# Optimization experiments

Hardware: AMD Instinct MI355X
Metric: run time of the kernel (lower is better)

Reference implementation:

```python
import jax, jax.numpy as jnp
import numpy as np

TEMP = 0.5
NUM_QUERIES = 256
NUM_NEGATIVES = 256
STRONG_THRESHOLD = 0.97


def _l2norm(x):
    n = jnp.sqrt(jnp.sum(x * x, axis=-1, keepdims=True))
    return x / jnp.maximum(n, 1e-12)


def _mls(mu0, mu1, s0, s1, w0, w1):
    # mutual likelihood score, mean over feature dim
    mu0 = _l2norm(mu0)
    mu1 = _l2norm(mu1)
    up = (mu0 * w0 - mu1 * w1) ** 2
    down = s0 * w0 + s1 * w1
    return -0.5 * jnp.mean(up / down + jnp.log(down), axis=-1)


def setup_inputs() -> dict:
    key = jax.random.key(0)
    B, C, H, W, S = 4, 32, 256, 256, 8
    ks = jax.random.split(key, 6)
    weights = jax.random.uniform(ks[0], (B, C, H, W), jnp.float32, 0.1, 1.0)
    mu = jax.random.normal(ks[1], (B, C, H, W), jnp.float32)
    sigma = jax.random.uniform(ks[2], (B, C, H, W), jnp.float32, 0.1, 1.0)
    cls = jax.random.randint(ks[3], (B, H, W), 0, S)
    label = jax.nn.one_hot(cls, S, axis=1, dtype=jnp.float32)  # [B,S,H,W]
    mask = (jax.random.uniform(ks[4], (B, 1, H, W)) < 0.7).astype(jnp.float32)
    prob = jax.random.uniform(ks[5], (B, S, H, W), jnp.float32)
    return {"weights": weights, "mu": mu, "sigma": sigma, "label": label, "mask": mask, "prob": prob}


def _rank_table(m, N):
    # m: bool [S, N]. table[s, r] = pixel index with rank r within class s.
    S = m.shape[0]
    ranks = jnp.cumsum(m, axis=1) - 1
    idx = jnp.where(m, ranks, N)  # out-of-range entries are dropped
    tbl = jnp.zeros((S, N), jnp.int32)
    rows = jnp.broadcast_to(jnp.arange(S)[:, None], (S, N))
    vals = jnp.broadcast_to(jnp.arange(N, dtype=jnp.int32)[None, :], (S, N))
    return tbl.at[rows, idx].set(vals, mode="drop")


def _forward(weights, mu, sigma, label, mask, prob):
    B, C, H, W = mu.shape
    S = label.shape[1]
    N = B * H * W
    Q, NEG = NUM_QUERIES, NUM_NEGATIVES
    mu_f = jnp.transpose(mu, (0, 2, 3, 1)).reshape(N, C)
    sig_f = jnp.transpose(sigma, (0, 2, 3, 1)).reshape(N, C)
    w_f = jnp.transpose(weights, (0, 2, 3, 1)).reshape(N, C)
    valid = jnp.transpose(label * mask, (1, 0, 2, 3)).reshape(S, N)  # [S,N]
    prob_f = jnp.transpose(prob, (1, 0, 2, 3)).reshape(S, N)
    vmask = valid > 0
    hmask = vmask & (prob_f < STRONG_THRESHOLD)
    count = jnp.sum(vmask, axis=1)
    hcount = jnp.sum(hmask, axis=1)
    # prototypes: masked sums over valid pixels (no_grad in original)
    inv_sig_w = w_f / sig_f
    proto_sigma = 1.0 / (valid @ inv_sig_w)                    # [S,C]
    proto_mu = proto_sigma * (valid @ (inv_sig_w * mu_f))      # [S,C]
    proto_weight = 1.0 / (valid @ (1.0 / w_f))                 # [S,C]
    proto_mu, proto_sigma, proto_weight = map(jax.lax.stop_gradient, (proto_mu, proto_sigma, proto_weight))
    tbl_valid = _rank_table(vmask, N)
    tbl_hard = _rank_table(hmask, N)
    keys = jax.random.split(jax.random.key(42), S)

    def per_class(i, key):
        k1, k2, k3 = jax.random.split(key, 3)
        # anchor sampling from hard pixels of class i (differentiable gather)
        ra = jnp.minimum((jax.random.uniform(k1, (Q,)) * hcount[i]).astype(jnp.int32), jnp.maximum(hcount[i] - 1, 0))
        apix = tbl_hard[i, ra]
        a_mu, a_sig, a_w = mu_f[apix], sig_f[apix], w_f[apix]
        # negative class distribution from prototype similarity
        order = (i + 1 + jnp.arange(S - 1)) % S
        sim = _mls(proto_mu[i][None], proto_mu[order], proto_sigma[i][None], proto_sigma[order], proto_weight[i][None], proto_weight[order])
        sim = jnp.where(count[order] > 0, sim, -jnp.inf)
        cls_pick = jax.random.categorical(k2, sim / TEMP, shape=(Q, NEG))
        neg_cls = order[cls_pick]                              # [Q,NEG]
        cnt = count[neg_cls]
        rn = jnp.minimum((jax.random.uniform(k3, (Q, NEG)) * cnt).astype(jnp.int32), jnp.maximum(cnt - 1, 0))
        npix = tbl_valid[neg_cls, rn]                          # [Q,NEG]
        n_mu = jax.lax.stop_gradient(mu_f[npix])
        n_sig = jax.lax.stop_gradient(sig_f[npix])
        n_w = jax.lax.stop_gradient(w_f[npix])
        pos_mu = jnp.broadcast_to(proto_mu[i], (Q, 1, C))
        pos_sig = jnp.broadcast_to(proto_sigma[i], (Q, 1, C))
        pos_w = jnp.broadcast_to(proto_weight[i], (Q, 1, C))
        all_mu = jnp.concatenate([pos_mu, n_mu], axis=1)       # [Q,1+NEG,C]
        all_sig = jnp.concatenate([pos_sig, n_sig], axis=1)
        all_w = jnp.concatenate([pos_w, n_w], axis=1)
        logits = _mls(a_mu[:, None], all_mu, a_sig[:, None], all_sig, a_w[:, None], all_w) / TEMP
        ce = jnp.mean(jax.nn.logsumexp(logits, axis=1) - logits[:, 0])
        ok = (hcount[i] > 0) & (count[i] > 0)
        return jnp.where(ok, ce, 0.0)

    losses = jax.vmap(per_class)(jnp.arange(S), keys)
    valid_num = jnp.sum(count > 0)
    return jnp.sum(losses) / valid_num.astype(losses.dtype)


def reference(weights, mu, sigma, label, mask, prob):
    return _forward(weights, mu, sigma, label, mask, prob)
```

## Files before the change

kernel.cpp:

```cpp
#include <hip/hip_runtime.h>
#include <hip/hip_fp16.h>
#include <stdint.h>


#define NPIX  262144
#define NCLS  8
#define NQ    256
#define NNEG  256
#define NBLK  1024

typedef unsigned short u16;
typedef unsigned int   u32;

struct TFKeys { u32 k1[8][2], k2[8][2], k3[8][2]; };

__host__ __device__ inline void tf2x32(u32 k0, u32 k1, u32 x0, u32 x1, u32& o0, u32& o1) {
  u32 ks2 = k0 ^ k1 ^ 0x1BD11BDAu;
  x0 += k0; x1 += k1;
#define TFR(R) { x0 += x1; x1 = (x1 << (R)) | (x1 >> (32 - (R))); x1 ^= x0; }
  TFR(13) TFR(15) TFR(26) TFR(6)
  x0 += k1;  x1 += ks2 + 1u;
  TFR(17) TFR(29) TFR(16) TFR(24)
  x0 += ks2; x1 += k0 + 2u;
  TFR(13) TFR(15) TFR(26) TFR(6)
  x0 += k0;  x1 += k1 + 3u;
  TFR(17) TFR(29) TFR(16) TFR(24)
  x0 += k1;  x1 += ks2 + 4u;
  TFR(13) TFR(15) TFR(26) TFR(6)
  x0 += ks2; x1 += k0 + 5u;
#undef TFR
  o0 = x0; o1 = x1;
}

__device__ inline float bfv(u16 v) { return __uint_as_float(((u32)v) << 16); }
__device__ inline float lo16(u32 v) { return __uint_as_float(v << 16); }
__device__ inline float hi16(u32 v) { return __uint_as_float(v & 0xFFFF0000u); }
__device__ inline float u01(u32 bits) { return __uint_as_float((bits >> 9) | 0x3F800000u) - 1.0f; }
__device__ inline u32 rbits(u32 k0, u32 k1, u32 idx) { u32 a, b; tf2x32(k0, k1, 0u, idx, a, b); return a ^ b; }
__device__ inline u32 packPQ(float p, float q) {
  return (u32)__half_as_ushort(__float2half(p)) | ((u32)__half_as_ushort(__float2half(q)) << 16);
}
__device__ inline float2 unpackPQ(u32 v) {
  return make_float2(__half2float(__ushort_as_half((u16)(v & 0xFFFFu))),
                     __half2float(__ushort_as_half((u16)(v >> 16))));
}
__device__ inline float frcp(float x) { return __builtin_amdgcn_rcpf(x); }

__global__ __launch_bounds__(256) void k_flags(const u16* __restrict__ lab, const u16* __restrict__ msk,
                                               const u16* __restrict__ prb, unsigned char* __restrict__ flags,
                                               int* __restrict__ blockCnt,
                                               float* __restrict__ protoAcc, float* __restrict__ ceAcc,
                                               int* __restrict__ diag) {
  __shared__ int cnt[16];
  int tid = threadIdx.x;
  if (blockIdx.x == 0) {
    for (int i = tid; i < 768; i += 256) protoAcc[i] = 0.f;
    if (tid < 8) ceAcc[tid] = 0.f;
    if (tid == 0) diag[0] = 0;
  }
  if (tid < 16) cnt[tid] = 0;
  __syncthreads();
  int n = blockIdx.x * 256 + tid;
  int b = n >> 16, hw = n & 65535;
  float m = bfv(msk[(b << 16) + hw]);
  int cls = 0; bool v = false;
  for (int s = 0; s < 8; s++) {
    float l = bfv(lab[((size_t)(b * 8 + s) << 16) + hw]);
    if (l * m > 0.f) { cls = s; v = true; }
  }
  bool h = false;
  if (v) { float p = bfv(prb[((size_t)(b * 8 + cls) << 16) + hw]); h = p < 0.97f; }
  flags[n] = (unsigned char)(cls | (v ? 16 : 0) | (h ? 32 : 0));
  if (v) atomicAdd(&cnt[cls], 1);
  if (h) atomicAdd(&cnt[8 + cls], 1);
  __syncthreads();
  if (tid < 16) blockCnt[tid * NBLK + blockIdx.x] = cnt[tid];
}

__global__ __launch_bounds__(256) void k_pq_proto(const u16* __restrict__ mu, const u16* __restrict__ wgt,
                                                  const u16* __restrict__ sig,
                                                  const unsigned char* __restrict__ flags,
                                                  u32* __restrict__ PQ, float* __restrict__ protoAcc) {
  __shared__ u32 tile[256 * 33];
  __shared__ float pacc[800];
  int t = threadIdx.x;
  pacc[t] = 0.f; pacc[t + 256] = 0.f; pacc[t + 512] = 0.f;
  if (t < 32) pacc[t + 768] = 0.f;
  __syncthreads();
  int n0 = blockIdx.x * 512;
  int b = n0 >> 16;
  int hwt = (n0 & 65535) + 2 * t;
  size_t cb = ((size_t)(b * 32)) << 16;
  u32 f2 = *(const u16*)(flags + n0 + 2 * t);
  int cls0 = (int)(f2 & 7u);         bool v0 = (f2 & 16u) != 0u;
  int cls1 = (int)((f2 >> 8) & 7u);  bool v1 = ((f2 >> 8) & 16u) != 0u;
  int base0 = cls0 * 100, base1 = cls1 * 100;
  u32 m2[32];
  float ss0 = 0.f, ss1 = 0.f;
  #pragma unroll
  for (int c = 0; c < 32; c++) {
    m2[c] = *(const u32*)(mu + cb + ((size_t)c << 16) + hwt);
    float a = lo16(m2[c]), d = hi16(m2[c]);
    ss0 += a * a; ss1 += d * d;
  }
  float rn0 = 1.0f / fmaxf(sqrtf(ss0), 1e-12f);
  float rn1 = 1.0f / fmaxf(sqrtf(ss1), 1e-12f);
  u32 pk0[32], pk1[32];
  #pragma unroll
  for (int c = 0; c < 32; c++) {
    u32 w2 = *(const u32*)(wgt + cb + ((size_t)c << 16) + hwt);
    u32 s2 = *(const u32*)(sig + cb + ((size_t)c << 16) + hwt);
    float wl = lo16(w2), wh = hi16(w2);
    float sl = lo16(s2), sh = hi16(s2);
    float ml = lo16(m2[c]), mh = hi16(m2[c]);
    pk0[c] = packPQ(ml * rn0 * wl, sl * wl);
    pk1[c] = packPQ(mh * rn1 * wh, sh * wh);
    if (v0) {
      float isw = wl / sl;
      atomicAdd(&pacc[base0 + c * 3 + 0], isw);
      atomicAdd(&pacc[base0 + c * 3 + 1], isw * ml);
      atomicAdd(&pacc[base0 + c * 3 + 2], 1.0f / wl);
    }
    if (v1) {
      float isw = wh / sh;
      atomicAdd(&pacc[base1 + c * 3 + 0], isw);
      atomicAdd(&pacc[base1 + c * 3 + 1], isw * mh);
      atomicAdd(&pacc[base1 + c * 3 + 2], 1.0f / wh);
    }
  }
  #pragma unroll
  for (int ch = 0; ch < 2; ch++) {
    if ((t >> 7) == ch) {
      int l = t & 127;
      #pragma unroll
      for (int c = 0; c < 32; c++) {
        tile[(2 * l + 0) * 33 + c] = pk0[c];
        tile[(2 * l + 1) * 33 + c] = pk1[c];
      }
    }
    __syncthreads();
    uint4* dst = (uint4*)(PQ + (size_t)(n0 + ch * 256) * 32);
    for (int k = t; k < 2048; k += 256) {
      int p = k >> 3, c4 = (k & 7) * 4;
      dst[k] = make_uint4(tile[p * 33 + c4], tile[p * 33 + c4 + 1],
                          tile[p * 33 + c4 + 2], tile[p * 33 + c4 + 3]);
    }
    __syncthreads();
  }
  for (int idx = t; idx < 800; idx += 256) {
    int cls = idx / 100, rem = idx - cls * 100;
    if (rem < 96) {
      int c = rem / 3, k = rem - c * 3;
      atomicAdd(&protoAcc[(cls * 32 + c) * 3 + k], pacc[idx]);
    }
  }
}

__global__ __launch_bounds__(256) void k_place(const unsigned char* __restrict__ flags,
                                               const int* __restrict__ blockCnt,
                                               int* __restrict__ tblV, int* __restrict__ tblH,
                                               int* __restrict__ counts) {
  __shared__ int wcnt[4][16];
  __shared__ int sOff[16], sTot[16];
  int tid = threadIdx.x;
  int blk = blockIdx.x;
  if (tid < 16) { sOff[tid] = 0; sTot[tid] = 0; }
  __syncthreads();
  {
    int ctr = tid & 15, seg = tid >> 4;
    const int* row = blockCnt + ctr * NBLK + seg * 64;
    int lim = blk - seg * 64;
    int pre = 0, tot = 0;
    #pragma unroll 8
    for (int l = 0; l < 64; ++l) {
      int v = row[l];
      tot += v;
      pre += (l < lim) ? v : 0;
    }
    atomicAdd(&sOff[ctr], pre);
    if (blk == 0) atomicAdd(&sTot[ctr], tot);
  }
  __syncthreads();
  if (blk == 0 && tid < 16) counts[tid] = sTot[tid];
  int n = blk * 256 + tid;
  int f = flags[n];
  int cls = f & 15; bool v = (f & 16) != 0, h = (f & 32) != 0;
  int wave = tid >> 6, lane = tid & 63;
  unsigned long long below = (1ull << lane) - 1ull;
  int rv = 0, rh = 0;
  for (int s = 0; s < 8; s++) {
    unsigned long long bv = __ballot(v && (cls == s));
    unsigned long long bh = __ballot(h && (cls == s));
    if (lane == 0) { wcnt[wave][s] = __popcll(bv); wcnt[wave][8 + s] = __popcll(bh); }
    if (cls == s) { rv = __popcll(bv & below); rh = __popcll(bh & below); }
  }
  __syncthreads();
  int preV = 0, preH = 0;
  for (int w2 = 0; w2 < wave; w2++) { preV += wcnt[w2][cls]; preH += wcnt[w2][8 + cls]; }
  if (v) tblV[(size_t)cls * NPIX + sOff[cls] + preV + rv] = n;
  if (h) tblH[(size_t)cls * NPIX + sOff[8 + cls] + preH + rh] = n;
}

__global__ void k_protoFinal(const float* __restrict__ protoAcc, const int* __restrict__ counts,
                             u32* __restrict__ protoPQ, float* __restrict__ simL,
                             int* __restrict__ diag) {
  __shared__ float sP[256], sQ[256];
  __shared__ int alive;
  int tid = threadIdx.x;
  if (tid == 0) alive = 0;
  float a0 = protoAcc[tid * 3 + 0], a1 = protoAcc[tid * 3 + 1], a2 = protoAcc[tid * 3 + 2];
  bool have = counts[tid >> 5] > 0;
  bool ok = (a0 > 0.f) && (a2 > 0.f);
  __syncthreads();
  if (have && !ok) atomicOr(diag, 2);
  if (have && ok) alive = 1;
  float psig = 1.0f / a0;
  float pmu  = psig * a1;
  float pw   = 1.0f / a2;
  float sq = (have && ok) ? pmu * pmu : 0.f;
  #pragma unroll
  for (int d = 1; d < 32; d <<= 1) sq += __shfl_xor(sq, d);
  float rn = 1.0f / fmaxf(sqrtf(sq), 1e-12f);
  float pP = (have && ok) ? pmu * rn * pw : 0.f;
  float pQ = (have && ok) ? psig * pw : 0.f;
  sP[tid] = pP; sQ[tid] = pQ;
  protoPQ[tid] = packPQ(pP, pQ);
  __syncthreads();
  if (tid == 0 && alive == 0) atomicOr(diag, 32);
  if (tid < 64) {
    int i = tid >> 3, j = tid & 7;
    if (j < 7) {
      int o = (i + 1 + j) & 7;
      float acc = 0.f;
      for (int c = 0; c < 32; c++) {
        float d = sP[i * 32 + c] - sP[o * 32 + c];
        float dn = sQ[i * 32 + c] + sQ[o * 32 + c];
        acc += d * d / dn + logf(dn);
      }
      float sim = -0.5f * (acc * (1.0f / 32.0f));
      simL[i * 8 + j] = (counts[o] > 0) ? (sim * 2.0f) : -INFINITY;
    }
  }
}

__global__ __launch_bounds__(256) void k_sample(TFKeys K, const float* __restrict__ simL,
                                                const int* __restrict__ counts,
                                                const int* __restrict__ tblV, const int* __restrict__ tblH,
                                                const u32* __restrict__ PQ, const u32* __restrict__ protoPQ,
                                                float* __restrict__ ceAcc, int* __restrict__ diag) {
  __shared__ float redM[4], redS[4];
  int blk = blockIdx.x;
  int i = blk >> 8, q = blk & 255;
  int t = threadIdx.x;
  u32 abits = rbits(K.k1[i][0], K.k1[i][1], (u32)q);
  float au = u01(abits);
  int hc = counts[8 + i];
  int ra = (int)(au * (float)hc);
  int cap = hc - 1; if (cap < 0) cap = 0;
  if (ra > cap) ra = cap; if (ra < 0) ra = 0;
  int ap = tblH[(size_t)i * NPIX + ra];
  if (ap < 0) ap = 0; if (ap > NPIX - 1) ap = NPIX - 1;
  const uint4* A4 = (const uint4*)(PQ + (size_t)ap * 32);
  u32 rem = (u32)(q * 256 + t);
  u32 k20 = K.k2[i][0], k21 = K.k2[i][1];
  float Lr[7];
  #pragma unroll
  for (int j = 0; j < 7; j++) Lr[j] = simL[i * 8 + j];
  float mg = 0.f; int pick = 0;
  #pragma unroll
  for (int j = 0; j < 7; j++) {
    u32 bits = rbits(k20, k21, rem * 7u + (u32)j);
    float f = u01(bits);
    float u = fmaxf(f, 1.17549435e-38f);
    float g = -__logf(-__logf(u));
    float v = g + Lr[j];
    if (j == 0) { mg = v; } else if (v > mg) { mg = v; pick = j; }
  }
  int nc = (i + 1 + pick) & 7;
  u32 bits3 = rbits(K.k3[i][0], K.k3[i][1], rem);
  float u3 = u01(bits3);
  int cntv = counts[nc];
  int rn = (int)(u3 * (float)cntv);
  int cap2 = cntv - 1; if (cap2 < 0) cap2 = 0;
  if (rn > cap2) rn = cap2; if (rn < 0) rn = 0;
  int np = tblV[(size_t)nc * NPIX + rn];
  if (np < 0) np = 0; if (np > NPIX - 1) np = NPIX - 1;
  const uint4* B = (const uint4*)(PQ + (size_t)np * 32);
  float accN = 0.f;
  #pragma unroll
  for (int k = 0; k < 8; k++) {
    uint4 ua = A4[k], ub = B[k];
    float2 fa, fb; float d, dn;
    fa = unpackPQ(ua.x); fb = unpackPQ(ub.x); d = fa.x - fb.x; dn = fa.y + fb.y; accN += d * d * frcp(dn) + __logf(dn);
    fa = unpackPQ(ua.y); fb = unpackPQ(ub.y); d = fa.x - fb.x; dn = fa.y + fb.y; accN += d * d * frcp(dn) + __logf(dn);
    fa = unpackPQ(ua.z); fb = unpackPQ(ub.z); d = fa.x - fb.x; dn = fa.y + fb.y; accN += d * d * frcp(dn) + __logf(dn);
    fa = unpackPQ(ua.w); fb = unpackPQ(ub.w); d = fa.x - fb.x; dn = fa.y + fb.y; accN += d * d * frcp(dn) + __logf(dn);
  }
  float lN = -(accN * (1.0f / 32.0f));
  float l0 = 0.f;
  if (t == 0) {
    const uint4* B0 = (const uint4*)(protoPQ + i * 32);
    float acc0 = 0.f;
    #pragma unroll
    for (int k = 0; k < 8; k++) {
      uint4 ua = A4[k], ub = B0[k];
      float2 fa, fb; float d, dn;
      fa = unpackPQ(ua.x); fb = unpackPQ(ub.x); d = fa.x - fb.x; dn = fa.y + fb.y; acc0 += d * d * frcp(dn) + __logf(dn);
      fa = unpackPQ(ua.y); fb = unpackPQ(ub.y); d = fa.x - fb.x; dn = fa.y + fb.y; acc0 += d * d * frcp(dn) + __logf(dn);
      fa = unpackPQ(ua.z); fb = unpackPQ(ub.z); d = fa.x - fb.x; dn = fa.y + fb.y; acc0 += d * d * frcp(dn) + __logf(dn);
      fa = unpackPQ(ua.w); fb = unpackPQ(ub.w); d = fa.x - fb.x; dn = fa.y + fb.y; acc0 += d * d * frcp(dn) + __logf(dn);
    }
    l0 = -(acc0 * (1.0f / 32.0f));
  }
  bool bad = !(lN == lN) || (t == 0 && !(l0 == l0));
  if (__ballot(bad) != 0ull && (t & 63) == 0) atomicOr(diag, 8);
  float lm = (t == 0) ? fmaxf(lN, l0) : lN;
  #pragma unroll
  for (int d = 1; d < 64; d <<= 1) lm = fmaxf(lm, __shfl_xor(lm, d));
  if ((t & 63) == 0) redM[t >> 6] = lm;
  __syncthreads();
  float M = fmaxf(fmaxf(redM[0], redM[1]), fmaxf(redM[2], redM[3]));
  float es = __expf(lN - M) + ((t == 0) ? __expf(l0 - M) : 0.f);
  #pragma unroll
  for (int d = 1; d < 64; d <<= 1) es += __shfl_xor(es, d);
  if ((t & 63) == 0) redS[t >> 6] = es;
  __syncthreads();
  if (t == 0) {
    float S = redS[0] + redS[1] + redS[2] + redS[3];
    float ce = (M + __logf(S)) - l0;
    atomicAdd(&ceAcc[i], ce);
  }
}

__global__ void k_final(const float* __restrict__ ceAcc, const int* __restrict__ counts,
                        const int* __restrict__ diag, u32* __restrict__ out) {
  if (blockIdx.x == 0 && threadIdx.x == 0) {
    float loss = 0.f; int vn = 0;
    int db = diag[0];
    for (int i = 0; i < 8; i++) {
      if (counts[i] > 0) vn++;
      float ce = ceAcc[i];
      if (counts[i] > 0 && counts[8 + i] > 0) {
        if (!(ce == ce)) db |= 4;
        loss += ce * (1.0f / 256.0f);
      }
    }
    if (vn == 0) db |= 1;
    loss = loss / (float)vn;
    if (!(loss == loss) && db == 0) db = 16;
    if (db != 0) loss = 4096.0f * (float)(1 + db);
    u32 fb = __float_as_uint(loss);
    u32 bv = (fb + 0x7FFFu + ((fb >> 16) & 1u)) >> 16;
    out[0] = (fb & 0xFFFF0000u) | (bv & 0xFFFFu);
  }
}

extern "C" void kernel_launch(void* const* d_in, const int* in_sizes, int n_in,
                              void* d_out, int out_size, void* d_ws, size_t ws_size,
                              hipStream_t stream) {
  (void)in_sizes; (void)n_in; (void)out_size; (void)ws_size;
  const u16* wgt = (const u16*)d_in[0];
  const u16* mu  = (const u16*)d_in[1];
  const u16* sig = (const u16*)d_in[2];
  const u16* lab = (const u16*)d_in[3];
  const u16* msk = (const u16*)d_in[4];
  const u16* prb = (const u16*)d_in[5];

  char* wp = (char*)d_ws;
  auto take = [&](size_t bytes) -> void* { void* p = (void*)wp; wp += ((bytes + 255) & ~(size_t)255); return p; };
  u32*   PQ       = (u32*)  take((size_t)NPIX * 32 * 4);
  int*   tblV     = (int*)  take((size_t)NCLS * NPIX * 4);
  int*   tblH     = (int*)  take((size_t)NCLS * NPIX * 4);
  unsigned char* flags = (unsigned char*)take(NPIX);
  int*   blockCnt = (int*)  take(16 * NBLK * 4);
  float* protoAcc = (float*)take(768 * 4);
  u32*   protoPQ  = (u32*)  take(256 * 4);
  float* simL     = (float*)take(64 * 4);
  int*   counts   = (int*)  take(16 * 4);
  float* ceAcc    = (float*)take(8 * 4);
  int*   diag     = (int*)  take(4);

  TFKeys K;
  for (u32 i = 0; i < 8; i++) {
    u32 ki0, ki1;
    tf2x32(0u, 42u, 0u, i, ki0, ki1);
    tf2x32(ki0, ki1, 0u, 0u, K.k1[i][0], K.k1[i][1]);
    tf2x32(ki0, ki1, 0u, 1u, K.k2[i][0], K.k2[i][1]);
    tf2x32(ki0, ki1, 0u, 2u, K.k3[i][0], K.k3[i][1]);
  }

  k_flags<<<1024, 256, 0, stream>>>(lab, msk, prb, flags, blockCnt, protoAcc, ceAcc, diag);
  k_pq_proto<<<512, 256, 0, stream>>>(mu, wgt, sig, flags, PQ, protoAcc);
  k_place<<<1024, 256, 0, stream>>>(flags, blockCnt, tblV, tblH, counts);
  k_protoFinal<<<1, 256, 0, stream>>>(protoAcc, counts, protoPQ, simL, diag);
  k_sample<<<2048, 256, 0, stream>>>(K, simL, counts, tblV, tblH, PQ, protoPQ, ceAcc, diag);
  k_final<<<1, 64, 0, stream>>>(ceAcc, counts, diag, (u32*)d_out);
}
```

Baseline: 227.6 us.

## Process one pixel per thread in pq_proto, writing PQ rows directly without LDS transpose

The prototype/PQ kernel now handles one pixel per thread instead of two. Each thread writes its packed 32-channel row to global memory directly as uint4 stores, so the shared-memory transpose tile and its barriers are gone, and the grid doubles to 1024 blocks. This frees LDS and registers for higher occupancy and removes sync overhead. In exchange the global loads become 2-byte scalar reads, mu is read twice, and the PQ stores are strided per thread (128 bytes apart) rather than coalesced.

```diff
diff --git a/kernel.cpp b/kernel.cpp
--- a/kernel.cpp
+++ b/kernel.cpp
@@ -81,78 +81,49 @@
                                                   const u16* __restrict__ sig,
                                                   const unsigned char* __restrict__ flags,
                                                   u32* __restrict__ PQ, float* __restrict__ protoAcc) {
-  __shared__ u32 tile[256 * 33];
   __shared__ float pacc[800];
   int t = threadIdx.x;
   pacc[t] = 0.f; pacc[t + 256] = 0.f; pacc[t + 512] = 0.f;
   if (t < 32) pacc[t + 768] = 0.f;
   __syncthreads();
-  int n0 = blockIdx.x * 512;
-  int b = n0 >> 16;
-  int hwt = (n0 & 65535) + 2 * t;
-  size_t cb = ((size_t)(b * 32)) << 16;
-  u32 f2 = *(const u16*)(flags + n0 + 2 * t);
-  int cls0 = (int)(f2 & 7u);         bool v0 = (f2 & 16u) != 0u;
-  int cls1 = (int)((f2 >> 8) & 7u);  bool v1 = ((f2 >> 8) & 16u) != 0u;
-  int base0 = cls0 * 100, base1 = cls1 * 100;
-  u32 m2[32];
-  float ss0 = 0.f, ss1 = 0.f;
+  int n = blockIdx.x * 256 + t;
+  int b = n >> 16, hw = n & 65535;
+  size_t cb = (((size_t)(b * 32)) << 16) + hw;
+  u32 f = flags[n];
+  int cls = (int)(f & 7u);
+  bool v = (f & 16u) != 0u;
+  int base = cls * 100;
+  float ss = 0.f;
   #pragma unroll
   for (int c = 0; c < 32; c++) {
-    m2[c] = *(const u32*)(mu + cb + ((size_t)c << 16) + hwt);
-    float a = lo16(m2[c]), d = hi16(m2[c]);
-    ss0 += a * a; ss1 += d * d;
-  }
-  float rn0 = 1.0f / fmaxf(sqrtf(ss0), 1e-12f);
-  float rn1 = 1.0f / fmaxf(sqrtf(ss1), 1e-12f);
-  u32 pk0[32], pk1[32];
-  #pragma unroll
-  for (int c = 0; c < 32; c++) {
-    u32 w2 = *(const u32*)(wgt + cb + ((size_t)c << 16) + hwt);
-    u32 s2 = *(const u32*)(sig + cb + ((size_t)c << 16) + hwt);
-    float wl = lo16(w2), wh = hi16(w2);
-    float sl = lo16(s2), sh = hi16(s2);
-    float ml = lo16(m2[c]), mh = hi16(m2[c]);
-    pk0[c] = packPQ(ml * rn0 * wl, sl * wl);
-    pk1[c] = packPQ(mh * rn1 * wh, sh * wh);
-    if (v0) {
-      float isw = wl / sl;
-      atomicAdd(&pacc[base0 + c * 3 + 0], isw);
-      atomicAdd(&pacc[base0 + c * 3 + 1], isw * ml);
-      atomicAdd(&pacc[base0 + c * 3 + 2], 1.0f / wl);
-    }
-    if (v1) {
-      float isw = wh / sh;
-      atomicAdd(&pacc[base1 + c * 3 + 0], isw);
-      atomicAdd(&pacc[base1 + c * 3 + 1], isw * mh);
-      atomicAdd(&pacc[base1 + c * 3 + 2], 1.0f / wh);
-    }
-  }
-  #pragma unroll
-  for (int ch = 0; ch < 2; ch++) {
-    if ((t >> 7) == ch) {
-      int l = t & 127;
-      #pragma unroll
-      for (int c = 0; c < 32; c++) {
-        tile[(2 * l + 0) * 33 + c] = pk0[c];
-        tile[(2 * l + 1) * 33 + c] = pk1[c];
+    float m = bfv(mu[cb + ((size_t)c << 16)]);
+    ss += m * m;
+  }
+  float rn = 1.0f / fmaxf(sqrtf(ss), 1e-12f);
+  uint4* dst = (uint4*)(PQ + (size_t)n * 32);
+  #pragma unroll
+  for (int k = 0; k < 8; k++) {
+    u32 pk[4];
+    #pragma unroll
+    for (int j = 0; j < 4; j++) {
+      int c = 4 * k + j;
+      float m = bfv(mu[cb + ((size_t)c << 16)]);
+      float w = bfv(wgt[cb + ((size_t)c << 16)]);
+      float s = bfv(sig[cb + ((size_t)c << 16)]);
+      pk[j] = packPQ(m * rn * w, s * w);
+      if (v) {
+        float isw = w / s;
+        atomicAdd(&pacc[base + c * 3 + 0], isw);
+        atomicAdd(&pacc[base + c * 3 + 1], isw * m);
+        atomicAdd(&pacc[base + c * 3 + 2], 1.0f / w);
       }
     }
-    __syncthreads();
-    uint4* dst = (uint4*)(PQ + (size_t)(n0 + ch * 256) * 32);
-    for (int k = t; k < 2048; k += 256) {
-      int p = k >> 3, c4 = (k & 7) * 4;
-      dst[k] = make_uint4(tile[p * 33 + c4], tile[p * 33 + c4 + 1],
-                          tile[p * 33 + c4 + 2], tile[p * 33 + c4 + 3]);
-    }
-    __syncthreads();
-  }
+    dst[k] = make_uint4(pk[0], pk[1], pk[2], pk[3]);
+  }
+  __syncthreads();
   for (int idx = t; idx < 800; idx += 256) {
-    int cls = idx / 100, rem = idx - cls * 100;
-    if (rem < 96) {
-      int c = rem / 3, k = rem - c * 3;
-      atomicAdd(&protoAcc[(cls * 32 + c) * 3 + k], pacc[idx]);
-    }
+    int c8 = idx / 100, rem = idx - c8 * 100;
+    if (rem < 96) atomicAdd(&protoAcc[c8 * 96 + rem], pacc[idx]);
   }
 }
 
@@ -390,7 +361,7 @@
   }
 
   k_flags<<<1024, 256, 0, stream>>>(lab, msk, prb, flags, blockCnt, protoAcc, ceAcc, diag);
-  k_pq_proto<<<512, 256, 0, stream>>>(mu, wgt, sig, flags, PQ, protoAcc);
+  k_pq_proto<<<1024, 256, 0, stream>>>(mu, wgt, sig, flags, PQ, protoAcc);
   k_place<<<1024, 256, 0, stream>>>(flags, blockCnt, tblV, tblH, counts);
   k_protoFinal<<<1, 256, 0, stream>>>(protoAcc, counts, protoPQ, simL, diag);
   k_sample<<<2048, 256, 0, stream>>>(K, simL, counts, tblV, tblH, PQ, protoPQ, ceAcc, diag);
```

Measured after the change: 252.4 us. 1.11x slower.
